# Kernel tuning notes

Measured on AMD Instinct MI355X. Metric: run time of the kernel, lower is better.

## Reference

```python
import jax, jax.numpy as jnp
import numpy as np

B_, S, D = 4, 4096, 2048   # batch, seq, d_model
OUT = 2048
E, R = 8, 16               # num_experts, lora rank
ALPHA = 32.0
SCALING = ALPHA / R


def setup_inputs() -> dict:
    key = jax.random.key(0)
    ks = jax.random.split(key, 6)
    x = jax.random.normal(ks[0], (B_, S, D), dtype=jnp.float32)
    W_base = jax.random.normal(ks[1], (OUT, D), dtype=jnp.float32) * (D ** -0.5)
    b_base = jax.random.normal(ks[2], (OUT,), dtype=jnp.float32) * 0.01
    router_W = jax.random.normal(ks[3], (E, D), dtype=jnp.float32) * (D ** -0.5)
    A = jax.random.normal(ks[4], (E, R, D), dtype=jnp.float32) * (D ** -0.5)   # lora_A weights [E, r, in]
    Bw = jax.random.normal(ks[5], (E, OUT, R), dtype=jnp.float32) * 0.02       # lora_B weights [E, out, r]
    return {"x": x, "W_base": W_base, "b_base": b_base, "router_W": router_W, "A": A, "Bw": Bw}


def reference(x, W_base, b_base, router_W, A, Bw):
    # frozen base linear
    base_out = jnp.einsum('bsd,od->bso', x, W_base) + b_base
    # router on detached input, top-1 expert
    logits = jnp.einsum('bsd,ed->bse', jax.lax.stop_gradient(x), router_W)
    routing_probs = jax.nn.softmax(logits, axis=-1)
    expert_idx = jnp.argmax(routing_probs, axis=-1)                 # [B,S]
    onehot = jax.nn.one_hot(expert_idx, E, dtype=x.dtype)           # [B,S,E]
    # LoRA down-proj for all experts (cheap: r=16), mask to selected expert
    h = jnp.einsum('bsd,erd->bser', x, A)                           # [B,S,E,R]
    h = h * onehot[..., None]
    # up-proj, combine over experts (only selected one is nonzero)
    delta = jnp.einsum('bser,eor->bso', h, Bw)                      # [B,S,OUT]
    return base_out + delta * SCALING
```

## Files before the change

kernel.cpp:

```cpp
#include <hip/hip_runtime.h>

#define D_    2048
#define OUT_  2048
#define E_    8
#define R_    16
#define KX    2176
#define M_    16384
#define SCALING_F 2.0f

typedef unsigned short ushort_t;
typedef unsigned short ushort8 __attribute__((ext_vector_type(8)));
typedef __bf16 bf16x8 __attribute__((ext_vector_type(8)));
typedef float f32x4 __attribute__((ext_vector_type(4)));

__device__ __forceinline__ ushort_t f2bf(float f) {
  unsigned u = __float_as_uint(f);
  u += 0x7FFFu + ((u >> 16) & 1u);
  return (ushort_t)(u >> 16);
}

#define GLOAD16(gp, lp)                                                        \
  __builtin_amdgcn_global_load_lds(                                            \
      (const __attribute__((address_space(1))) void*)(gp),                     \
      (__attribute__((address_space(3))) void*)(lp), 16, 0, 0)

__global__ __launch_bounds__(256) void wprep_all_kernel(
    const float* __restrict__ W, const float* __restrict__ Bw,
    const float* __restrict__ A,
    ushort_t* __restrict__ wext, ushort_t* __restrict__ aext)
{
  const int bid = blockIdx.x;
  const int t = threadIdx.x;
  if (bid < OUT_) {
    const int o = bid;
    const float* wr = W + (size_t)o * D_ + t * 8;
    float4 v0 = *(const float4*)wr;
    float4 v1 = *(const float4*)(wr + 4);
    ushort8 wb;
    wb[0] = f2bf(v0.x); wb[1] = f2bf(v0.y); wb[2] = f2bf(v0.z); wb[3] = f2bf(v0.w);
    wb[4] = f2bf(v1.x); wb[5] = f2bf(v1.y); wb[6] = f2bf(v1.z); wb[7] = f2bf(v1.w);
    *(ushort8*)(wext + (size_t)o * KX + t * 8) = wb;
    if (t < E_ * R_) {
      const int e = t >> 4, r = t & 15;
      wext[(size_t)o * KX + D_ + t] = f2bf(Bw[((size_t)e * OUT_ + o) * R_ + r]);
    }
  } else {
    const size_t i = ((size_t)(bid - OUT_) * 256 + t) * 8;
    float4 v0 = *(const float4*)(A + i);
    float4 v1 = *(const float4*)(A + i + 4);
    ushort8 b;
    b[0] = f2bf(v0.x); b[1] = f2bf(v0.y); b[2] = f2bf(v0.z); b[3] = f2bf(v0.w);
    b[4] = f2bf(v1.x); b[5] = f2bf(v1.y); b[6] = f2bf(v1.z); b[7] = f2bf(v1.w);
    *(ushort8*)(aext + i) = b;
  }
}

__global__ __launch_bounds__(256) void router_kernel(
    const float* __restrict__ x, const float* __restrict__ rW,
    int* __restrict__ eidx)
{
  const int t = threadIdx.x, lane = t & 63, wid = t >> 6;
  const int m0 = (blockIdx.x * 4 + wid) * 4;

  float acc[4][E_];
  #pragma unroll
  for (int k = 0; k < 4; ++k)
    #pragma unroll
    for (int e = 0; e < E_; ++e) acc[k][e] = 0.f;

  #pragma unroll
  for (int j = 0; j < 8; ++j) {
    const int col = j * 256 + lane * 4;
    float4 w[E_];
    #pragma unroll
    for (int e = 0; e < E_; ++e)
      w[e] = *(const float4*)(rW + (size_t)e * D_ + col);
    #pragma unroll
    for (int k = 0; k < 4; ++k) {
      float4 xv = *(const float4*)(x + (size_t)(m0 + k) * D_ + col);
      #pragma unroll
      for (int e = 0; e < E_; ++e)
        acc[k][e] += xv.x * w[e].x + xv.y * w[e].y + xv.z * w[e].z + xv.w * w[e].w;
    }
  }

  #pragma unroll
  for (int k = 0; k < 4; ++k) {
    float r[E_];
    #pragma unroll
    for (int e = 0; e < E_; ++e) r[e] = acc[k][e];
    #pragma unroll
    for (int off = 1; off <= 4; off <<= 1)
      #pragma unroll
      for (int e = 0; e < E_; ++e) r[e] += __shfl_xor(r[e], off, 64);
    double s[E_];
    #pragma unroll
    for (int e = 0; e < E_; ++e) s[e] = (double)r[e];
    #pragma unroll
    for (int off = 8; off <= 32; off <<= 1)
      #pragma unroll
      for (int e = 0; e < E_; ++e) s[e] += __shfl_xor(s[e], off, 64);
    int bi = 0; double best = s[0];
    #pragma unroll
    for (int e = 1; e < E_; ++e)
      if (s[e] > best) { best = s[e]; bi = e; }
    if (lane == 0) eidx[m0 + k] = bi;
  }
}

#define HG_NKT (D_ / 64)

__global__ __launch_bounds__(256) void hgemm_kernel(
    const float* __restrict__ x,
    const ushort_t* __restrict__ Ae,
    const int* __restrict__ eidx,
    ushort_t* __restrict__ xext)
{
  __shared__ __attribute__((aligned(16))) char lds[40960];

  const int t = threadIdx.x;
  const int lane = t & 63, w = t >> 6;
  const int wr = w >> 1, wc = w & 1;
  const int lr = lane & 15, lg = lane >> 4;
  const int koff = (lr & 7) << 4;

  const int bm = blockIdx.x;
  const size_t row0 = (size_t)bm * 32;

  const int sg_row = t >> 3;
  const int sg_c = t & 7;
  const int sg_slotx = sg_c ^ (sg_row & 7);

  auto stageA = [&](int TT) {
    char* dst = lds + (TT & 1) * 20480 + 4096;
    #pragma unroll
    for (int g = 0; g < 4; ++g) {
      const int r = g * 32 + sg_row;
      GLOAD16(Ae + (size_t)r * D_ + TT * 64 + sg_slotx * 8,
              dst + g * 4096 + t * 16);
    }
  };
  auto putX = [&](int TT, const float4& a, const float4& b) {
    ushort8 xb;
    xb[0] = f2bf(a.x); xb[1] = f2bf(a.y); xb[2] = f2bf(a.z); xb[3] = f2bf(a.w);
    xb[4] = f2bf(b.x); xb[5] = f2bf(b.y); xb[6] = f2bf(b.z); xb[7] = f2bf(b.w);
    char* Xb = lds + (TT & 1) * 20480;
    *(ushort8*)(Xb + sg_row * 128 + sg_slotx * 16) = xb;
    *(ushort8*)(xext + (row0 + sg_row) * KX + TT * 64 + sg_c * 8) = xb;
  };

  f32x4 acc[4] = {};

  {
    const float* xp = x + (row0 + sg_row) * D_ + sg_c * 8;
    float4 a = *(const float4*)xp;
    float4 b = *(const float4*)(xp + 4);
    stageA(0);
    putX(0, a, b);
  }
  __syncthreads();

  for (int T = 0; T < HG_NKT; ++T) {
    float4 na, nb;
    const bool more = (T + 1 < HG_NKT);
    if (more) {
      const float* xp = x + (row0 + sg_row) * D_ + (T + 1) * 64 + sg_c * 8;
      na = *(const float4*)xp;
      nb = *(const float4*)(xp + 4);
      stageA(T + 1);
    }
    char* Xb = lds + (T & 1) * 20480;
    char* Ab = Xb + 4096;
    bf16x8 af[2], bfr[4][2];
    #pragma unroll
    for (int kk = 0; kk < 2; ++kk)
      af[kk] = *(const bf16x8*)(Xb + (wr * 16 + lr) * 128 + ((kk * 64 + lg * 16) ^ koff));
    #pragma unroll
    for (int nj = 0; nj < 4; ++nj) {
      const int R = wc * 64 + nj * 16 + lr;
      #pragma unroll
      for (int kk = 0; kk < 2; ++kk)
        bfr[nj][kk] = *(const bf16x8*)(Ab + R * 128 + ((kk * 64 + lg * 16) ^ koff));
    }
    #pragma unroll
    for (int nj = 0; nj < 4; ++nj)
      #pragma unroll
      for (int kk = 0; kk < 2; ++kk)
        acc[nj] = __builtin_amdgcn_mfma_f32_16x16x32_bf16(af[kk], bfr[nj][kk], acc[nj], 0, 0, 0);
    if (more) putX(T + 1, na, nb);
    __syncthreads();
  }

  int er[4];
  #pragma unroll
  for (int rr = 0; rr < 4; ++rr)
    er[rr] = eidx[row0 + wr * 16 + lg * 4 + rr];
  #pragma unroll
  for (int nj = 0; nj < 4; ++nj) {
    const int col = wc * 64 + nj * 16 + lr;
    const int ecol = wc * 4 + nj;
    #pragma unroll
    for (int rr = 0; rr < 4; ++rr) {
      const size_t row = row0 + wr * 16 + lg * 4 + rr;
      ushort_t v = (er[rr] == ecol) ? f2bf(acc[nj][rr] * SCALING_F) : (ushort_t)0;
      xext[row * KX + D_ + col] = v;
    }
  }
}

#define NKT (KX / 64)
#define NITER (NKT / 2)
#define NSTG (NKT * 4)

__global__ __launch_bounds__(512, 2) void gemm_kernel(
    const ushort_t* __restrict__ Ag,
    const ushort_t* __restrict__ Bg,
    const float* __restrict__ bias,
    float* __restrict__ C)
{
  __shared__ __attribute__((aligned(16))) char lds[131072];

  const int t = threadIdx.x;
  const int lane = t & 63, w = t >> 6;
  const int wm = w >> 2, wn = w & 3;
  const int lr = lane & 15, lg = lane >> 4;
  const int koff = (lr & 7) << 4;

  const int swz = (blockIdx.x & 7) * 64 + (blockIdx.x >> 3);
  const int bm = swz >> 3, bn = swz & 7;

  const int sg_row = t >> 3;
  const int sg_slotx = (t & 7) ^ ((t >> 3) & 7);
  const size_t aRow0 = (size_t)bm * 256;
  const size_t bRow0 = (size_t)bn * 256;

  auto stage = [&](int s) {
    if (s >= NSTG) return;
    const int TT = s >> 2, j = s & 3;
    const int isB = j >> 1, half = j & 1;
    const ushort_t* src = isB ? Bg : Ag;
    const size_t gr0 = (isB ? bRow0 : aRow0) + half * 128;
    char* dst = lds + (TT & 1) * 65536 + isB * 32768 + half * 16384;
    #pragma unroll
    for (int g = 0; g < 2; ++g) {
      const int r = g * 64 + sg_row;
      GLOAD16(src + (gr0 + r) * KX + TT * 64 + sg_slotx * 8,
              dst + g * 8192 + t * 16);
    }
  };

  f32x4 acc[8][4] = {};
  bf16x8 bq[4][2];

  stage(0); stage(1); stage(2); stage(3);
  stage(6); stage(7);
  asm volatile("s_waitcnt vmcnt(4)" ::: "memory");
  __builtin_amdgcn_s_barrier();

  for (int ii = 0; ii < NITER; ++ii) {
    #pragma unroll
    for (int p = 0; p < 8; ++p) {
      const int q = p & 3;
      char* Ab = lds + ((2 * ii + (p >> 2)) & 1) * 65536;
      char* Bb = Ab + 32768;
      bf16x8 aq[2][2];
      if (q == 0) {
        #pragma unroll
        for (int nj = 0; nj < 4; ++nj) {
          const int R = wn * 64 + nj * 16 + lr;
          #pragma unroll
          for (int kk = 0; kk < 2; ++kk)
            bq[nj][kk] = *(const bf16x8*)(Bb + R * 128 + ((kk * 64 + lg * 16) ^ koff));
        }
      }
      #pragma unroll
      for (int i = 0; i < 2; ++i) {
        const int R = wm * 128 + (q * 2 + i) * 16 + lr;
        #pragma unroll
        for (int kk = 0; kk < 2; ++kk)
          aq[i][kk] = *(const bf16x8*)(Ab + R * 128 + ((kk * 64 + lg * 16) ^ koff));
      }
      switch (p) {
        case 0: stage(4 * (2 * ii + 1) + 0); break;
        case 1: stage(4 * (2 * ii + 1) + 1); break;
        case 2: stage(4 * (2 * ii + 2) + 2); break;
        case 3: stage(4 * (2 * ii + 2) + 3); break;
        case 4: stage(4 * (2 * ii + 2) + 0); break;
        case 5: stage(4 * (2 * ii + 2) + 1); break;
        case 6: stage(4 * (2 * ii + 3) + 2); break;
        case 7: stage(4 * (2 * ii + 3) + 3); break;
      }
      if (q == 0) asm volatile("s_waitcnt lgkmcnt(8)" ::: "memory");
      __builtin_amdgcn_s_barrier();
      asm volatile("s_waitcnt lgkmcnt(0)" ::: "memory");
      __builtin_amdgcn_s_setprio(1);
      #pragma unroll
      for (int i = 0; i < 2; ++i)
        #pragma unroll
        for (int nj = 0; nj < 4; ++nj)
          #pragma unroll
          for (int kk = 0; kk < 2; ++kk)
            acc[q * 2 + i][nj] = __builtin_amdgcn_mfma_f32_16x16x32_bf16(
                aq[i][kk], bq[nj][kk], acc[q * 2 + i][nj], 0, 0, 0);
      __builtin_amdgcn_s_setprio(0);
      if (p == 3 || p == 7) {
        if (ii == NITER - 1) asm volatile("s_waitcnt vmcnt(0)" ::: "memory");
        else                 asm volatile("s_waitcnt vmcnt(4)" ::: "memory");
      }
      __builtin_amdgcn_s_barrier();
    }
  }

  #pragma unroll
  for (int nj = 0; nj < 4; ++nj) {
    const int col = bn * 256 + wn * 64 + nj * 16 + lr;
    const float bv = bias[col];
    #pragma unroll
    for (int mi = 0; mi < 8; ++mi) {
      const int row0 = bm * 256 + wm * 128 + mi * 16 + lg * 4;
      #pragma unroll
      for (int rr = 0; rr < 4; ++rr)
        C[(size_t)(row0 + rr) * OUT_ + col] = acc[mi][nj][rr] + bv;
    }
  }
}

extern "C" void kernel_launch(void* const* d_in, const int* in_sizes, int n_in,
                              void* d_out, int out_size, void* d_ws, size_t ws_size,
                              hipStream_t stream) {
  const float* x  = (const float*)d_in[0];
  const float* Wb = (const float*)d_in[1];
  const float* bb = (const float*)d_in[2];
  const float* rW = (const float*)d_in[3];
  const float* A  = (const float*)d_in[4];
  const float* Bw = (const float*)d_in[5];
  float* out = (float*)d_out;

  ushort_t* xext = (ushort_t*)d_ws;
  ushort_t* wext = (ushort_t*)((char*)d_ws + (size_t)M_ * KX * 2);
  int* eidx = (int*)((char*)d_ws + (size_t)M_ * KX * 2 + (size_t)OUT_ * KX * 2);
  ushort_t* aext = (ushort_t*)((char*)eidx + M_ * sizeof(int));

  wprep_all_kernel<<<OUT_ + (E_ * R_ * D_) / (256 * 8), 256, 0, stream>>>(Wb, Bw, A, wext, aext);
  router_kernel<<<M_ / 16, 256, 0, stream>>>(x, rW, eidx);
  hgemm_kernel<<<M_ / 32, 256, 0, stream>>>(x, aext, eidx, xext);
  gemm_kernel<<<(M_ / 256) * (OUT_ / 256), 512, 0, stream>>>(xext, wext, bb, out);
}
```

Measured before the change: 247.4 us.

## Fuse router logit computation into the LoRA down-projection kernel

Removes the separate router kernel and computes the router logits inside the hgemm kernel from the x values it already loads for bf16 conversion. The argmax is reduced across the 8 lanes sharing a row and passed through shared memory, so the global eidx buffer and one full read of x are no longer needed. The cost is extra per-thread FMA work and router-weight loads inside the main loop, plus register pressure from eight accumulators. Summation order also changes, which could flip argmax on near-ties.

```diff
diff --git a/kernel.cpp b/kernel.cpp
--- a/kernel.cpp
+++ b/kernel.cpp
@@ -55,68 +55,16 @@
   }
 }
 
-__global__ __launch_bounds__(256) void router_kernel(
-    const float* __restrict__ x, const float* __restrict__ rW,
-    int* __restrict__ eidx)
-{
-  const int t = threadIdx.x, lane = t & 63, wid = t >> 6;
-  const int m0 = (blockIdx.x * 4 + wid) * 4;
-
-  float acc[4][E_];
-  #pragma unroll
-  for (int k = 0; k < 4; ++k)
-    #pragma unroll
-    for (int e = 0; e < E_; ++e) acc[k][e] = 0.f;
-
-  #pragma unroll
-  for (int j = 0; j < 8; ++j) {
-    const int col = j * 256 + lane * 4;
-    float4 w[E_];
-    #pragma unroll
-    for (int e = 0; e < E_; ++e)
-      w[e] = *(const float4*)(rW + (size_t)e * D_ + col);
-    #pragma unroll
-    for (int k = 0; k < 4; ++k) {
-      float4 xv = *(const float4*)(x + (size_t)(m0 + k) * D_ + col);
-      #pragma unroll
-      for (int e = 0; e < E_; ++e)
-        acc[k][e] += xv.x * w[e].x + xv.y * w[e].y + xv.z * w[e].z + xv.w * w[e].w;
-    }
-  }
-
-  #pragma unroll
-  for (int k = 0; k < 4; ++k) {
-    float r[E_];
-    #pragma unroll
-    for (int e = 0; e < E_; ++e) r[e] = acc[k][e];
-    #pragma unroll
-    for (int off = 1; off <= 4; off <<= 1)
-      #pragma unroll
-      for (int e = 0; e < E_; ++e) r[e] += __shfl_xor(r[e], off, 64);
-    double s[E_];
-    #pragma unroll
-    for (int e = 0; e < E_; ++e) s[e] = (double)r[e];
-    #pragma unroll
-    for (int off = 8; off <= 32; off <<= 1)
-      #pragma unroll
-      for (int e = 0; e < E_; ++e) s[e] += __shfl_xor(s[e], off, 64);
-    int bi = 0; double best = s[0];
-    #pragma unroll
-    for (int e = 1; e < E_; ++e)
-      if (s[e] > best) { best = s[e]; bi = e; }
-    if (lane == 0) eidx[m0 + k] = bi;
-  }
-}
-
 #define HG_NKT (D_ / 64)
 
-__global__ __launch_bounds__(256) void hgemm_kernel(
+__global__ __launch_bounds__(256) void hrouter_kernel(
     const float* __restrict__ x,
+    const float* __restrict__ rW,
     const ushort_t* __restrict__ Ae,
-    const int* __restrict__ eidx,
     ushort_t* __restrict__ xext)
 {
   __shared__ __attribute__((aligned(16))) char lds[40960];
+  __shared__ int esel[32];
 
   const int t = threadIdx.x;
   const int lane = t & 63, w = t >> 6;
@@ -149,6 +97,20 @@
     *(ushort8*)(xext + (row0 + sg_row) * KX + TT * 64 + sg_c * 8) = xb;
   };
 
+  float la[E_];
+  #pragma unroll
+  for (int e = 0; e < E_; ++e) la[e] = 0.f;
+  auto accLogit = [&](int TT, const float4& a, const float4& b) {
+    const float* wp = rW + TT * 64 + sg_c * 8;
+    #pragma unroll
+    for (int e = 0; e < E_; ++e) {
+      float4 w0 = *(const float4*)(wp + (size_t)e * D_);
+      float4 w1 = *(const float4*)(wp + (size_t)e * D_ + 4);
+      la[e] += a.x * w0.x + a.y * w0.y + a.z * w0.z + a.w * w0.w
+             + b.x * w1.x + b.y * w1.y + b.z * w1.z + b.w * w1.w;
+    }
+  };
+
   f32x4 acc[4] = {};
 
   {
@@ -157,6 +119,7 @@
     float4 b = *(const float4*)(xp + 4);
     stageA(0);
     putX(0, a, b);
+    accLogit(0, a, b);
   }
   __syncthreads();
 
@@ -187,14 +150,33 @@
       #pragma unroll
       for (int kk = 0; kk < 2; ++kk)
         acc[nj] = __builtin_amdgcn_mfma_f32_16x16x32_bf16(af[kk], bfr[nj][kk], acc[nj], 0, 0, 0);
-    if (more) putX(T + 1, na, nb);
+    if (more) {
+      putX(T + 1, na, nb);
+      accLogit(T + 1, na, nb);
+    }
     __syncthreads();
   }
+
+  {
+    double s[E_];
+    #pragma unroll
+    for (int e = 0; e < E_; ++e) s[e] = (double)la[e];
+    #pragma unroll
+    for (int off = 1; off <= 4; off <<= 1)
+      #pragma unroll
+      for (int e = 0; e < E_; ++e) s[e] += __shfl_xor(s[e], off, 64);
+    int bi = 0; double best = s[0];
+    #pragma unroll
+    for (int e = 1; e < E_; ++e)
+      if (s[e] > best) { best = s[e]; bi = e; }
+    if (sg_c == 0) esel[sg_row] = bi;
+  }
+  __syncthreads();
 
   int er[4];
   #pragma unroll
   for (int rr = 0; rr < 4; ++rr)
-    er[rr] = eidx[row0 + wr * 16 + lg * 4 + rr];
+    er[rr] = esel[wr * 16 + lg * 4 + rr];
   #pragma unroll
   for (int nj = 0; nj < 4; ++nj) {
     const int col = wc * 64 + nj * 16 + lr;
@@ -338,11 +320,10 @@
 
   ushort_t* xext = (ushort_t*)d_ws;
   ushort_t* wext = (ushort_t*)((char*)d_ws + (size_t)M_ * KX * 2);
-  int* eidx = (int*)((char*)d_ws + (size_t)M_ * KX * 2 + (size_t)OUT_ * KX * 2);
-  ushort_t* aext = (ushort_t*)((char*)eidx + M_ * sizeof(int));
+  ushort_t* aext = (ushort_t*)((char*)d_ws + (size_t)M_ * KX * 2
+                                           + (size_t)OUT_ * KX * 2);
 
   wprep_all_kernel<<<OUT_ + (E_ * R_ * D_) / (256 * 8), 256, 0, stream>>>(Wb, Bw, A, wext, aext);
-  router_kernel<<<M_ / 16, 256, 0, stream>>>(x, rW, eidx);
-  hgemm_kernel<<<M_ / 32, 256, 0, stream>>>(x, aext, eidx, xext);
+  hrouter_kernel<<<M_ / 32, 256, 0, stream>>>(x, rW, aext, xext);
   gemm_kernel<<<(M_ / 256) * (OUT_ / 256), 512, 0, stream>>>(xext, wext, bb, out);
 }
```

Result: faster. 238.1 us, median of 2 (-3.8%).
